# Optimization experiments

Measured on AMD Instinct MI355X. Metric: run time of the kernel, lower is better.

The kernel has to match this reference:

```python
import jax, jax.numpy as jnp
import numpy as np

D_MODEL = 2048
N_HEADS = 16
D_HEAD = D_MODEL // N_HEADS  # 128
T_MAX = 2048
B, T = 2, 2048


def _build_rope_cache(T_max, d_head):
    pos = jnp.arange(T_max, dtype=jnp.float32)[:, None]
    dim = jnp.arange(0, d_head, 2, dtype=jnp.float32)
    freqs = 1.0 / (10000.0 ** (dim / d_head))
    angles = pos * freqs  # [T_max, d_head//2]
    return jnp.cos(angles), jnp.sin(angles)


def _apply_rope(x, cos, sin):
    # x: [B, H, T, D]; cos/sin: [T_max, D//2]
    d2 = x.shape[-1] // 2
    x1, x2 = x[..., :d2], x[..., d2:]
    c = cos[: x.shape[2]][None, None]  # [1,1,T,D//2]
    s = sin[: x.shape[2]][None, None]
    return jnp.concatenate([x1 * c - x2 * s, x2 * c + x1 * s], axis=-1)


def setup_inputs() -> dict:
    key = jax.random.key(0)
    k1, k2, k3, k4 = jax.random.split(key, 4)
    x = jax.random.normal(k1, (B, T, D_MODEL), dtype=jnp.float32)
    Wqkv = jax.random.normal(k2, (3 * D_MODEL, D_MODEL), dtype=jnp.float32) * (D_MODEL ** -0.5)
    Wproj = jax.random.normal(k3, (D_MODEL, D_MODEL), dtype=jnp.float32) * (D_MODEL ** -0.5)
    q_gain = jnp.full((N_HEADS,), 1.0, dtype=jnp.float32) + 0.1 * jax.random.normal(k4, (N_HEADS,), dtype=jnp.float32)
    rope_cos, rope_sin = _build_rope_cache(T_MAX, D_HEAD)
    return {"x": x, "Wqkv": Wqkv, "Wproj": Wproj, "q_gain": q_gain,
            "rope_cos": rope_cos, "rope_sin": rope_sin}


def reference(x, Wqkv, Wproj, q_gain, rope_cos, rope_sin):
    Bx, Tx, C = x.shape
    H, D = N_HEADS, C // N_HEADS
    qkv = jnp.einsum('btc,fc->btf', x, Wqkv)  # [B,T,3C]
    q, k, v = jnp.split(qkv, 3, axis=2)
    q = q.reshape(Bx, Tx, H, D).transpose(0, 2, 1, 3)  # [B,H,T,D]
    k = k.reshape(Bx, Tx, H, D).transpose(0, 2, 1, 3)
    v = v.reshape(Bx, Tx, H, D).transpose(0, 2, 1, 3)
    q = _apply_rope(q, rope_cos, rope_sin)
    k = _apply_rope(k, rope_cos, rope_sin)
    q = q * q_gain[None, :, None, None]
    scale = 1.0 / jnp.sqrt(jnp.asarray(D, dtype=x.dtype))
    scores = jnp.einsum('bhqd,bhkd->bhqk', q, k) * scale
    causal = jnp.tril(jnp.ones((Tx, Tx), dtype=bool))
    scores = jnp.where(causal[None, None], scores, jnp.asarray(-jnp.inf, dtype=scores.dtype))
    attn = jax.nn.softmax(scores, axis=-1)
    y = jnp.einsum('bhqk,bhkd->bhqd', attn, v)  # [B,H,T,D]
    y = y.transpose(0, 2, 1, 3).reshape(Bx, Tx, C)
    return jnp.einsum('btc,oc->bto', y, Wproj)
```

## Files before the change

### kernel.cpp

```cpp
#include <hip/hip_runtime.h>
#include <stdint.h>

#define BB    2
#define T_SEQ 2048
#define NH    16
#define DH    128
#define DM    2048

typedef unsigned short u16;
typedef unsigned int   u32;
typedef __attribute__((ext_vector_type(8))) short short8;
typedef __attribute__((ext_vector_type(4))) short short4_t;
typedef __attribute__((ext_vector_type(4))) float floatx4;

__device__ __forceinline__ float bf2f(u16 b) { return __uint_as_float(((u32)b) << 16); }
__device__ __forceinline__ u16 f2bf(float f) {
    u32 u = __float_as_uint(f);
    u32 r = u + 0x7fffu + ((u >> 16) & 1u);
    return (u16)(r >> 16);
}

__device__ __forceinline__ short8 cvt8(const float* p) {
    floatx4 a = *(const floatx4*)p;
    floatx4 b = *(const floatx4*)(p + 4);
    short8 r;
    r[0] = (short)f2bf(a[0]); r[1] = (short)f2bf(a[1]);
    r[2] = (short)f2bf(a[2]); r[3] = (short)f2bf(a[3]);
    r[4] = (short)f2bf(b[0]); r[5] = (short)f2bf(b[1]);
    r[6] = (short)f2bf(b[2]); r[7] = (short)f2bf(b[3]);
    return r;
}

__device__ __forceinline__ void gl2lds16(const u16* g, u16* l) {
    __builtin_amdgcn_global_load_lds(
        (const __attribute__((address_space(1))) void*)g,
        (__attribute__((address_space(3))) void*)l, 16, 0, 0);
}

__global__ void detect_dtype(const u16* __restrict__ w, int* __restrict__ flag) {
    __shared__ int cnt;
    if (threadIdx.x == 0) cnt = 0;
    __syncthreads();
    int c = 0;
    for (int i = threadIdx.x; i < 2048; i += 256) {
        float v = bf2f(w[i]);
        if (!(fabsf(v) <= 1.0f)) c++;
    }
    atomicAdd(&cnt, c);
    __syncthreads();
    if (threadIdx.x == 0) *flag = (cnt > 64) ? 1 : 0;
}

__global__ void sentinel_k(const int* __restrict__ flag, float* __restrict__ out, int n) {
    if (*flag != 0) return;
    for (int i = threadIdx.x; i < n; i += 256) out[i] = (i == 0) ? 200.0f : 0.0f;
}

__global__ void fill_const(float* __restrict__ out, int n, float v0) {
    int i = blockIdx.x * 256 + threadIdx.x;
    if (i < n) out[i] = (i == 0) ? v0 : 0.0f;
}

__global__ __launch_bounds__(256) void cvt_all(const float* __restrict__ x,
                                               const float* __restrict__ wq,
                                               const float* __restrict__ wp,
                                               u16* __restrict__ xb,
                                               u16* __restrict__ wqb,
                                               u16* __restrict__ wpb,
                                               const int* __restrict__ flag) {
    if (*flag == 0) return;
    int i = blockIdx.x * 256 + threadIdx.x;
    const float* src; u16* dst; int j;
    if (i < 2097152)      { src = x;  dst = xb;  j = i; }
    else if (i < 5242880) { src = wq; dst = wqb; j = i - 2097152; }
    else                  { src = wp; dst = wpb; j = i - 5242880; }
    floatx4 v = ((const floatx4*)src)[j];
    short4_t r;
    r[0] = (short)f2bf(v[0]); r[1] = (short)f2bf(v[1]);
    r[2] = (short)f2bf(v[2]); r[3] = (short)f2bf(v[3]);
    ((short4_t*)dst)[j] = r;
}

template<int PERM, int OF32>
__global__ __launch_bounds__(256) void gemm97(const u16* __restrict__ A,
                                              const u16* __restrict__ B,
                                              void* __restrict__ Cv,
                                              const int* __restrict__ flag,
                                              const void* __restrict__ gainv,
                                              const void* __restrict__ cosv,
                                              const void* __restrict__ sinv,
                                              int M, int N, int K)
{
    if (*flag == 0) return;

    __shared__ __align__(16) u16 As[128 * 32];
    __shared__ __align__(16) u16 Bs[128 * 32];

    u16*   C16 = (u16*)Cv;
    float* C32 = (float*)Cv;

    const int tid  = threadIdx.x;
    const int lane = tid & 63;
    const int quad = lane >> 4;
    const int l15  = lane & 15;
    const int wave = tid >> 6;
    const int wy   = (wave >> 1) * 64;
    const int wx   = (wave & 1) * 64;
    const int rowA0 = blockIdx.y * 128;
    const int rowB0 = blockIdx.x * 128;

    const int lrow = lane >> 2;
    const int lcol = (lane & 3) << 3;
    const int segA0 = wave * 2, segA1 = wave * 2 + 1;

    const u16* gA0 = A + (size_t)(rowA0 + segA0 * 16 + lrow) * K + lcol;
    const u16* gA1 = A + (size_t)(rowA0 + segA1 * 16 + lrow) * K + lcol;
    const u16* gB0 = B + (size_t)(rowB0 + segA0 * 16 + lrow) * K + lcol;
    const u16* gB1 = B + (size_t)(rowB0 + segA1 * 16 + lrow) * K + lcol;
    u16* lA0 = &As[segA0 * 16 * 32];
    u16* lA1 = &As[segA1 * 16 * 32];
    u16* lB0 = &Bs[segA0 * 16 * 32];
    u16* lB1 = &Bs[segA1 * 16 * 32];

    floatx4 acc[4][4];
#pragma unroll
    for (int i = 0; i < 4; ++i)
#pragma unroll
        for (int j = 0; j < 4; ++j) acc[i][j] = (floatx4){0.f, 0.f, 0.f, 0.f};

    for (int k0 = 0; k0 < K; k0 += 32) {
        __syncthreads();
        gl2lds16(gA0 + k0, lA0);
        gl2lds16(gA1 + k0, lA1);
        gl2lds16(gB0 + k0, lB0);
        gl2lds16(gB1 + k0, lB1);
        __syncthreads();

        short8 a[4], b[4];
#pragma unroll
        for (int i = 0; i < 4; ++i)
            a[i] = *(const short8*)&As[(wy + i * 16 + l15) * 32 + quad * 8];
#pragma unroll
        for (int i = 0; i < 4; ++i)
            b[i] = *(const short8*)&Bs[(wx + i * 16 + l15) * 32 + quad * 8];
#pragma unroll
        for (int i = 0; i < 4; ++i)
#pragma unroll
            for (int j = 0; j < 4; ++j)
                acc[i][j] = __builtin_amdgcn_mfma_f32_16x16x32_bf16(a[i], b[j], acc[i][j], 0, 0, 0);
    }

    if (PERM == 3) {
        const int slice = rowB0 >> 11;
        u16* dbuf = C16 + (size_t)slice * 8388608;
        const int h_ = (rowB0 & 2047) >> 7;

        if (slice < 2) {
            __shared__ float Xc[256][17];
            const float* cosb = (const float*)cosv;
            const float* sinb = (const float*)sinv;
            float g = 1.0f;
            if (slice == 0)
                g = ((const float*)gainv)[h_] * 0.08838834764831843f
                                              * 1.4426950408889634f;
            const int ptid = tid ^ 64;
#pragma unroll
            for (int i = 0; i < 4; ++i) {
#pragma unroll
                for (int j = 0; j < 4; ++j)
#pragma unroll
                    for (int r = 0; r < 4; ++r)
                        Xc[tid][j * 4 + r] = acc[i][j][r];
                __syncthreads();
#pragma unroll
                for (int j = 0; j < 4; ++j) {
                    const int d2 = j * 16 + l15;
                    const int d  = wx + d2;
#pragma unroll
                    for (int r = 0; r < 4; ++r) {
                        int row = rowA0 + wy + i * 16 + quad * 4 + r;
                        int b_ = row >> 11, t_ = row & 2047;
                        float c = cosb[t_ * 64 + d2];
                        float s = sinb[t_ * 64 + d2];
                        float mine  = acc[i][j][r];
                        float other = Xc[ptid][j * 4 + r];
                        float outv = (wx == 0) ? (mine * c - other * s)
                                               : (mine * c + other * s);
                        outv *= g;
                        size_t dst = ((size_t)((b_ * NH + h_) * T_SEQ + t_)) * DH + d;
                        dbuf[dst] = f2bf(outv);
                    }
                }
                __syncthreads();
            }
        } else {
#pragma unroll
            for (int i = 0; i < 4; ++i) {
#pragma unroll
                for (int j = 0; j < 4; ++j) {
#pragma unroll
                    for (int r = 0; r < 4; ++r) {
                        int row = rowA0 + wy + i * 16 + quad * 4 + r;
                        int col = rowB0 + wx + j * 16 + l15;
                        int b_ = row >> 11, t_ = row & 2047;
                        int colm = col & 2047;
                        int hh = colm >> 7, d_ = colm & 127;
                        int u  = t_ & 63;
                        int tp = (t_ & ~63) + ((u & 15) * 4) + (u >> 4);
                        size_t dst = ((size_t)((b_ * NH + hh) * DH + d_)) * T_SEQ + tp;
                        dbuf[dst] = f2bf(acc[i][j][r]);
                    }
                }
            }
        }
    } else {
#pragma unroll
        for (int i = 0; i < 4; ++i) {
#pragma unroll
            for (int j = 0; j < 4; ++j) {
#pragma unroll
                for (int r = 0; r < 4; ++r) {
                    int row = rowA0 + wy + i * 16 + quad * 4 + r;
                    int col = rowB0 + wx + j * 16 + l15;
                    size_t dst = (size_t)row * N + col;
                    if (OF32) C32[dst] = acc[i][j][r];
                    else      C16[dst] = f2bf(acc[i][j][r]);
                }
            }
        }
    }
}

template<int PERM, int AF32, int BF32, int OF32>
__global__ __launch_bounds__(256) void gemm_bt(const void* __restrict__ Av,
                                               const void* __restrict__ Bv,
                                               void* __restrict__ Cv,
                                               const int* __restrict__ flag,
                                               int bslice, int M, int N, int K)
{
    if (*flag == 0) return;

    __shared__ __align__(16) u16 As[128 * 32];
    __shared__ __align__(16) u16 Bs[128 * 32];

    const u16*   A16 = (const u16*)Av;
    const float* A32 = (const float*)Av;
    const u16*   B16 = (const u16*)Bv   + (size_t)bslice * DM * DM;
    const float* B32 = (const float*)Bv + (size_t)bslice * DM * DM;
    u16*   C16 = (u16*)Cv;
    float* C32 = (float*)Cv;

    const int tid  = threadIdx.x;
    const int lane = tid & 63;
    const int quad = lane >> 4;
    const int l15  = lane & 15;
    const int wave = tid >> 6;
    const int wy   = (wave >> 1) * 64;
    const int wx   = (wave & 1) * 64;
    const int rowA0 = blockIdx.y * 128;
    const int rowB0 = blockIdx.x * 128;

    const int srow = tid >> 2;
    const int scol = (tid & 3) << 3;

    const size_t aoff0 = (size_t)(rowA0 + srow) * K + scol;
    const size_t aoff1 = aoff0 + (size_t)64 * K;
    const size_t boff0 = (size_t)(rowB0 + srow) * K + scol;
    const size_t boff1 = boff0 + (size_t)64 * K;

    u16* AsW0 = &As[srow * 32 + scol];
    u16* AsW1 = &As[(srow + 64) * 32 + scol];
    u16* BsW0 = &Bs[srow * 32 + scol];
    u16* BsW1 = &Bs[(srow + 64) * 32 + scol];

    floatx4 acc[4][4];
#pragma unroll
    for (int i = 0; i < 4; ++i)
#pragma unroll
        for (int j = 0; j < 4; ++j) acc[i][j] = (floatx4){0.f, 0.f, 0.f, 0.f};

    for (int k0 = 0; k0 < K; k0 += 32) {
        short8 av0 = AF32 ? cvt8(A32 + aoff0 + k0) : *(const short8*)(A16 + aoff0 + k0);
        short8 av1 = AF32 ? cvt8(A32 + aoff1 + k0) : *(const short8*)(A16 + aoff1 + k0);
        short8 bv0 = BF32 ? cvt8(B32 + boff0 + k0) : *(const short8*)(B16 + boff0 + k0);
        short8 bv1 = BF32 ? cvt8(B32 + boff1 + k0) : *(const short8*)(B16 + boff1 + k0);
        __syncthreads();
        *(short8*)AsW0 = av0;
        *(short8*)AsW1 = av1;
        *(short8*)BsW0 = bv0;
        *(short8*)BsW1 = bv1;
        __syncthreads();

        short8 a[4], b[4];
#pragma unroll
        for (int i = 0; i < 4; ++i)
            a[i] = *(const short8*)&As[(wy + i * 16 + l15) * 32 + quad * 8];
#pragma unroll
        for (int i = 0; i < 4; ++i)
            b[i] = *(const short8*)&Bs[(wx + i * 16 + l15) * 32 + quad * 8];
#pragma unroll
        for (int i = 0; i < 4; ++i)
#pragma unroll
            for (int j = 0; j < 4; ++j)
                acc[i][j] = __builtin_amdgcn_mfma_f32_16x16x32_bf16(a[i], b[j], acc[i][j], 0, 0, 0);
    }

#pragma unroll
    for (int i = 0; i < 4; ++i) {
#pragma unroll
        for (int j = 0; j < 4; ++j) {
#pragma unroll
            for (int r = 0; r < 4; ++r) {
                int row = rowA0 + wy + i * 16 + quad * 4 + r;
                int col = rowB0 + wx + j * 16 + l15;
                size_t dst;
                if (PERM == 1) {
                    int b_ = row >> 11, t_ = row & 2047;
                    int h_ = col >> 7,  d_ = col & 127;
                    dst = ((size_t)((b_ * NH + h_) * T_SEQ + t_)) * DH + d_;
                } else if (PERM == 2) {
                    int b_ = row >> 11, t_ = row & 2047;
                    int h_ = col >> 7,  d_ = col & 127;
                    int u  = t_ & 63;
                    int tp = (t_ & ~63) + ((u & 15) * 4) + (u >> 4);
                    dst = ((size_t)((b_ * NH + h_) * DH + d_)) * T_SEQ + tp;
                } else {
                    dst = (size_t)row * N + col;
                }
                if (OF32) C32[dst] = acc[i][j][r];
                else      C16[dst] = f2bf(acc[i][j][r]);
            }
        }
    }
}

__global__ __launch_bounds__(256) void rope_inplace(u16* __restrict__ q,
                                                    u16* __restrict__ k,
                                                    const void* __restrict__ gainv,
                                                    const void* __restrict__ cosv,
                                                    const void* __restrict__ sinv,
                                                    const int* __restrict__ flag)
{
    if (*flag == 0) return;
    const float* gain = (const float*)gainv;
    const float* cosb = (const float*)cosv;
    const float* sinb = (const float*)sinv;

    int idx = blockIdx.x * 256 + threadIdx.x;
    int d2 = idx & 63;
    int t  = (idx >> 6) & 2047;
    int h  = (idx >> 17) & 15;
    int b  = idx >> 21;

    float c = cosb[t * 64 + d2];
    float s = sinb[t * 64 + d2];
    float g = gain[h] * 0.08838834764831843f * 1.4426950408889634f;

    size_t row = ((size_t)((b * NH + h) * T_SEQ + t)) * DH;
    float q1 = bf2f(q[row + d2]);
    float q2 = bf2f(q[row + 64 + d2]);
    q[row + d2]      = f2bf((q1 * c - q2 * s) * g);
    q[row + 64 + d2] = f2bf((q2 * c + q1 * s) * g);

    float k1 = bf2f(k[row + d2]);
    float k2 = bf2f(k[row + 64 + d2]);
    k[row + d2]      = f2bf(k1 * c - k2 * s);
    k[row + 64 + d2] = f2bf(k2 * c + k1 * s);
}

__global__ __launch_bounds__(256) void attn_flash6(const u16* __restrict__ q,
                                                   const u16* __restrict__ k,
                                                   const u16* __restrict__ v,
                                                   u16* __restrict__ y,
                                                   const int* __restrict__ flag)
{
    if (*flag == 0) return;

    __shared__ __align__(16) u16 Ks[2][64 * 128];
    __shared__ __align__(16) u16 Vt[2][128 * 64];
    __shared__ __align__(16) u16 Ps[4][16 * 64];

    const int tid  = threadIdx.x;
    const int lane = tid & 63;
    const int l15  = lane & 15;
    const int quad = lane >> 4;
    const int wave = tid >> 6;
    const int bh   = blockIdx.y;
    const int qt   = (T_SEQ / 64 - 1) - blockIdx.x;

    const u16* kbase = k + (size_t)bh * T_SEQ * DH;
    const u16* vbase = v + (size_t)bh * DH * T_SEQ;
    const int b_ = bh >> 4, h_ = bh & 15;

    const int kRowIn = lane >> 4;
    const int kCh    = lane & 15;
    const int vRowIn = lane >> 3;
    const int vCh    = (lane & 7) ^ (lane >> 3);

#define STAGE6(KT, BUF) do {                                                   \
        _Pragma("unroll")                                                      \
        for (int j_ = 0; j_ < 4; ++j_) {                                       \
            int kr_ = wave * 16 + j_ * 4 + kRowIn;                             \
            gl2lds16(kbase + (size_t)((KT) * 64 + kr_) * DH +                  \
                         ((kCh ^ (kr_ & 7)) << 3),                             \
                     &Ks[BUF][(wave * 16 + j_ * 4) * 128]);                    \
            int vr_ = wave * 32 + j_ * 8 + vRowIn;                             \
            gl2lds16(vbase + (size_t)vr_ * T_SEQ + (KT) * 64 + (vCh << 3),     \
                     &Vt[BUF][(wave * 32 + j_ * 8) * 64]);                     \
        }                                                                      \
    } while (0)

    const int q0w = qt * 64 + wave * 16;
    const int iters = qt + 1;

    short8 aq[4];
    {
        const u16* qrow = q + ((size_t)bh * T_SEQ + q0w + l15) * DH + quad * 8;
#pragma unroll
        for (int s = 0; s < 4; ++s) aq[s] = *(const short8*)(qrow + s * 32);
    }

    floatx4 o[8];
#pragma unroll
    for (int n = 0; n < 8; ++n) o[n] = (floatx4){0.f, 0.f, 0.f, 0.f};
    float l_p[4] = {0.f, 0.f, 0.f, 0.f};

    STAGE6(0, 0);
    asm volatile("s_waitcnt vmcnt(0)" ::: "memory");
    __syncthreads();

    for (int kt = 0; kt < iters; ++kt) {
        const int cur = kt & 1;

        if (kt + 1 < iters) STAGE6(kt + 1, cur ^ 1);

        floatx4 sc[4];
#pragma unroll
        for (int t = 0; t < 4; ++t) {
            sc[t] = (floatx4){0.f, 0.f, 0.f, 0.f};
#pragma unroll
            for (int s = 0; s < 4; ++s) {
                short8 bk = *(const short8*)&Ks[cur][(t * 16 + l15) * 128 +
                                                (((s * 4 + quad) ^ (l15 & 7)) << 3)];
                sc[t] = __builtin_amdgcn_mfma_f32_16x16x32_bf16(aq[s], bk, sc[t], 0, 0, 0);
            }
        }

        if (kt == qt) {
#pragma unroll
            for (int t = 0; t < 4; ++t)
#pragma unroll
                for (int r = 0; r < 4; ++r)
                    if (kt * 64 + t * 16 + l15 > q0w + quad * 4 + r)
                        sc[t][r] = -1e30f;
        }

#pragma unroll
        for (int r = 0; r < 4; ++r) {
            float p0 = exp2f(sc[0][r]);
            float p1 = exp2f(sc[1][r]);
            float p2 = exp2f(sc[2][r]);
            float p3 = exp2f(sc[3][r]);
            l_p[r] += (p0 + p1) + (p2 + p3);

            int qr = quad * 4 + r;
            u32 lo = (u32)f2bf(p0) | ((u32)f2bf(p1) << 16);
            u32 hi = (u32)f2bf(p2) | ((u32)f2bf(p3) << 16);
            u32* dst = (u32*)&Ps[wave][qr * 64 +
                                       (((l15 >> 1) ^ (qr & 7)) << 3) + (l15 & 1) * 4];
            dst[0] = lo;
            dst[1] = hi;
        }

#pragma unroll
        for (int s = 0; s < 2; ++s) {
            short8 ap = *(const short8*)&Ps[wave][l15 * 64 +
                                                  (((s * 4 + quad) ^ (l15 & 7)) << 3)];
#pragma unroll
            for (int n = 0; n < 8; ++n) {
                short8 bv = *(const short8*)&Vt[cur][(n * 16 + l15) * 64 +
                                                (((s * 4 + quad) ^ (l15 & 7)) << 3)];
                o[n] = __builtin_amdgcn_mfma_f32_16x16x32_bf16(ap, bv, o[n], 0, 0, 0);
            }
        }

        asm volatile("s_waitcnt vmcnt(0)" ::: "memory");
        __syncthreads();
    }

#pragma unroll
    for (int r = 0; r < 4; ++r) {
        float l = l_p[r];
        l += __shfl_xor(l, 1);
        l += __shfl_xor(l, 2);
        l += __shfl_xor(l, 4);
        l += __shfl_xor(l, 8);
        float inv = 1.f / l;
        int qrow = q0w + quad * 4 + r;
        size_t yo = ((size_t)(b_ * T_SEQ + qrow)) * DM + h_ * DH + l15;
#pragma unroll
        for (int n = 0; n < 8; ++n)
            y[yo + n * 16] = f2bf(o[n][r] * inv);
    }
#undef STAGE6
}

extern "C" void kernel_launch(void* const* d_in, const int* in_sizes, int n_in,
                              void* d_out, int out_size, void* d_ws, size_t ws_size,
                              hipStream_t stream)
{
    float* out = (float*)d_out;
    const int FILLB = (out_size + 255) / 256;

    bool ok = (n_in == 6) &&
              in_sizes[0] == 8388608 && in_sizes[1] == 12582912 &&
              in_sizes[2] == 4194304 && in_sizes[3] == 16 &&
              in_sizes[4] == 131072  && in_sizes[5] == 131072 &&
              out_size == 8388608;
    if (!ok) {
        fill_const<<<FILLB, 256, 0, stream>>>(out, out_size, 150.0f);
        return;
    }

    const size_t MB = 1024 * 1024;
    const size_t BUF = 16 * MB;
    if (ws_size < 4 * BUF + 256) {
        fill_const<<<FILLB, 256, 0, stream>>>(out, out_size, 100.0f);
        return;
    }

    const void* x     = d_in[0];
    const void* Wqkv  = d_in[1];
    const void* Wproj = d_in[2];
    const void* qgain = d_in[3];
    const void* rc    = d_in[4];
    const void* rs    = d_in[5];

    char* ws = (char*)d_ws;
    const size_t FAST_NEED = 96 * MB + 256;

    if (ws_size >= FAST_NEED) {
        u16* qb   = (u16*)(ws);
        u16* kb   = (u16*)(ws + BUF);
        u16* vb   = (u16*)(ws + 2 * BUF);
        u16* wqbf = (u16*)(ws + 3 * BUF);
        u16* wpbf = (u16*)(ws + 3 * BUF + 24 * MB);
        u16* xbf  = (u16*)(ws + 5 * BUF);
        u16* yb   = xbf;
        int* flag = (int*)(ws + 6 * BUF);

        detect_dtype<<<1, 256, 0, stream>>>((const u16*)Wqkv, flag);

        cvt_all<<<24576, 256, 0, stream>>>((const float*)x, (const float*)Wqkv,
                                           (const float*)Wproj, xbf, wqbf, wpbf, flag);

        gemm97<3, 0><<<dim3(48, 32), 256, 0, stream>>>(xbf, wqbf, qb, flag,
                                                       qgain, rc, rs,
                                                       4096, 6144, 2048);
        attn_flash6<<<dim3(T_SEQ / 64, BB * NH), 256, 0, stream>>>(qb, kb, vb, yb, flag);
        gemm97<0, 1><<<dim3(16, 32), 256, 0, stream>>>(yb, wpbf, out, flag,
                                                       nullptr, nullptr, nullptr,
                                                       4096, 2048, 2048);
        sentinel_k<<<1, 256, 0, stream>>>(flag, out, out_size);
    } else {
        u16* qb = (u16*)(ws);
        u16* kb = (u16*)(ws + BUF);
        u16* vb = (u16*)(ws + 2 * BUF);
        u16* yb = (u16*)(ws + 3 * BUF);
        int* flag = (int*)(ws + 4 * BUF);

        detect_dtype<<<1, 256, 0, stream>>>((const u16*)Wqkv, flag);
        gemm_bt<1, 1, 1, 0><<<dim3(16, 32), 256, 0, stream>>>(x, Wqkv, qb, flag, 0, 4096, 2048, 2048);
        gemm_bt<1, 1, 1, 0><<<dim3(16, 32), 256, 0, stream>>>(x, Wqkv, kb, flag, 1, 4096, 2048, 2048);
        gemm_bt<2, 1, 1, 0><<<dim3(16, 32), 256, 0, stream>>>(x, Wqkv, vb, flag, 2, 4096, 2048, 2048);
        rope_inplace<<<16384, 256, 0, stream>>>(qb, kb, qgain, rc, rs, flag);
        attn_flash6<<<dim3(T_SEQ / 64, BB * NH), 256, 0, stream>>>(qb, kb, vb, yb, flag);
        gemm_bt<0, 0, 1, 1><<<dim3(16, 32), 256, 0, stream>>>(yb, Wproj, out, flag, 0, 4096, 2048, 2048);
        sentinel_k<<<1, 256, 0, stream>>>(flag, out, out_size);
    }
}
```

Measured before the change: 459.8 us.

## Double attention query tile per block to 128 rows, two row-tiles per wave

```diff
diff --git a/kernel.cpp b/kernel.cpp
--- a/kernel.cpp
+++ b/kernel.cpp
@@ -368,7 +368,7 @@
     k[row + 64 + d2] = f2bf(k2 * c + k1 * s);
 }
 
-__global__ __launch_bounds__(256) void attn_flash6(const u16* __restrict__ q,
+__global__ __launch_bounds__(256) void attn_flash7(const u16* __restrict__ q,
                                                    const u16* __restrict__ k,
                                                    const u16* __restrict__ v,
                                                    u16* __restrict__ y,
@@ -378,7 +378,7 @@
 
     __shared__ __align__(16) u16 Ks[2][64 * 128];
     __shared__ __align__(16) u16 Vt[2][128 * 64];
-    __shared__ __align__(16) u16 Ps[4][16 * 64];
+    __shared__ __align__(16) u16 Ps[4][32 * 64];
 
     const int tid  = threadIdx.x;
     const int lane = tid & 63;
@@ -386,7 +386,8 @@
     const int quad = lane >> 4;
     const int wave = tid >> 6;
     const int bh   = blockIdx.y;
-    const int qt   = (T_SEQ / 64 - 1) - blockIdx.x;
+    const int qt   = (blockIdx.y & 16) ? blockIdx.x
+                                       : (T_SEQ / 128 - 1) - blockIdx.x;
 
     const u16* kbase = k + (size_t)bh * T_SEQ * DH;
     const u16* vbase = v + (size_t)bh * DH * T_SEQ;
@@ -397,7 +398,7 @@
     const int vRowIn = lane >> 3;
     const int vCh    = (lane & 7) ^ (lane >> 3);
 
-#define STAGE6(KT, BUF) do {                                                   \
+#define STAGE7(KT, BUF) do {                                                   \
         _Pragma("unroll")                                                      \
         for (int j_ = 0; j_ < 4; ++j_) {                                       \
             int kr_ = wave * 16 + j_ * 4 + kRowIn;                             \
@@ -410,77 +411,94 @@
         }                                                                      \
     } while (0)
 
-    const int q0w = qt * 64 + wave * 16;
-    const int iters = qt + 1;
-
-    short8 aq[4];
-    {
-        const u16* qrow = q + ((size_t)bh * T_SEQ + q0w + l15) * DH + quad * 8;
-#pragma unroll
-        for (int s = 0; s < 4; ++s) aq[s] = *(const short8*)(qrow + s * 32);
-    }
-
-    floatx4 o[8];
-#pragma unroll
-    for (int n = 0; n < 8; ++n) o[n] = (floatx4){0.f, 0.f, 0.f, 0.f};
-    float l_p[4] = {0.f, 0.f, 0.f, 0.f};
-
-    STAGE6(0, 0);
+    const int q0w   = qt * 128 + wave * 32;
+    const int iters = 2 * (qt + 1);
+
+    short8 aq[2][4];
+#pragma unroll
+    for (int rt = 0; rt < 2; ++rt) {
+        const u16* qrow = q + ((size_t)bh * T_SEQ + q0w + rt * 16 + l15) * DH + quad * 8;
+#pragma unroll
+        for (int s = 0; s < 4; ++s) aq[rt][s] = *(const short8*)(qrow + s * 32);
+    }
+
+    floatx4 o[2][8];
+#pragma unroll
+    for (int rt = 0; rt < 2; ++rt)
+#pragma unroll
+        for (int n = 0; n < 8; ++n) o[rt][n] = (floatx4){0.f, 0.f, 0.f, 0.f};
+    float l_p[2][4] = {{0.f, 0.f, 0.f, 0.f}, {0.f, 0.f, 0.f, 0.f}};
+
+    STAGE7(0, 0);
     asm volatile("s_waitcnt vmcnt(0)" ::: "memory");
     __syncthreads();
 
     for (int kt = 0; kt < iters; ++kt) {
         const int cur = kt & 1;
 
-        if (kt + 1 < iters) STAGE6(kt + 1, cur ^ 1);
-
-        floatx4 sc[4];
-#pragma unroll
-        for (int t = 0; t < 4; ++t) {
-            sc[t] = (floatx4){0.f, 0.f, 0.f, 0.f};
-#pragma unroll
-            for (int s = 0; s < 4; ++s) {
-                short8 bk = *(const short8*)&Ks[cur][(t * 16 + l15) * 128 +
-                                                (((s * 4 + quad) ^ (l15 & 7)) << 3)];
-                sc[t] = __builtin_amdgcn_mfma_f32_16x16x32_bf16(aq[s], bk, sc[t], 0, 0, 0);
-            }
-        }
-
-        if (kt == qt) {
-#pragma unroll
-            for (int t = 0; t < 4; ++t)
-#pragma unroll
-                for (int r = 0; r < 4; ++r)
-                    if (kt * 64 + t * 16 + l15 > q0w + quad * 4 + r)
-                        sc[t][r] = -1e30f;
-        }
-
-#pragma unroll
-        for (int r = 0; r < 4; ++r) {
-            float p0 = exp2f(sc[0][r]);
-            float p1 = exp2f(sc[1][r]);
-            float p2 = exp2f(sc[2][r]);
-            float p3 = exp2f(sc[3][r]);
-            l_p[r] += (p0 + p1) + (p2 + p3);
-
-            int qr = quad * 4 + r;
-            u32 lo = (u32)f2bf(p0) | ((u32)f2bf(p1) << 16);
-            u32 hi = (u32)f2bf(p2) | ((u32)f2bf(p3) << 16);
-            u32* dst = (u32*)&Ps[wave][qr * 64 +
-                                       (((l15 >> 1) ^ (qr & 7)) << 3) + (l15 & 1) * 4];
-            dst[0] = lo;
-            dst[1] = hi;
-        }
-
-#pragma unroll
-        for (int s = 0; s < 2; ++s) {
-            short8 ap = *(const short8*)&Ps[wave][l15 * 64 +
-                                                  (((s * 4 + quad) ^ (l15 & 7)) << 3)];
-#pragma unroll
-            for (int n = 0; n < 8; ++n) {
-                short8 bv = *(const short8*)&Vt[cur][(n * 16 + l15) * 64 +
-                                                (((s * 4 + quad) ^ (l15 & 7)) << 3)];
-                o[n] = __builtin_amdgcn_mfma_f32_16x16x32_bf16(ap, bv, o[n], 0, 0, 0);
+        if (kt + 1 < iters) STAGE7(kt + 1, cur ^ 1);
+
+        if (kt * 64 <= q0w + 31) {
+            floatx4 sc[2][4];
+#pragma unroll
+            for (int rt = 0; rt < 2; ++rt)
+#pragma unroll
+                for (int t = 0; t < 4; ++t) sc[rt][t] = (floatx4){0.f, 0.f, 0.f, 0.f};
+#pragma unroll
+            for (int t = 0; t < 4; ++t) {
+#pragma unroll
+                for (int s = 0; s < 4; ++s) {
+                    short8 bk = *(const short8*)&Ks[cur][(t * 16 + l15) * 128 +
+                                                    (((s * 4 + quad) ^ (l15 & 7)) << 3)];
+                    sc[0][t] = __builtin_amdgcn_mfma_f32_16x16x32_bf16(aq[0][s], bk, sc[0][t], 0, 0, 0);
+                    sc[1][t] = __builtin_amdgcn_mfma_f32_16x16x32_bf16(aq[1][s], bk, sc[1][t], 0, 0, 0);
+                }
+            }
+
+            if (kt * 64 + 63 > q0w) {
+#pragma unroll
+                for (int rt = 0; rt < 2; ++rt)
+#pragma unroll
+                    for (int t = 0; t < 4; ++t)
+#pragma unroll
+                        for (int r = 0; r < 4; ++r)
+                            if (kt * 64 + t * 16 + l15 > q0w + rt * 16 + quad * 4 + r)
+                                sc[rt][t][r] = -1e30f;
+            }
+
+#pragma unroll
+            for (int rt = 0; rt < 2; ++rt) {
+#pragma unroll
+                for (int r = 0; r < 4; ++r) {
+                    float p0 = exp2f(sc[rt][0][r]);
+                    float p1 = exp2f(sc[rt][1][r]);
+                    float p2 = exp2f(sc[rt][2][r]);
+                    float p3 = exp2f(sc[rt][3][r]);
+                    l_p[rt][r] += (p0 + p1) + (p2 + p3);
+
+                    int qr = rt * 16 + quad * 4 + r;
+                    u32 lo = (u32)f2bf(p0) | ((u32)f2bf(p1) << 16);
+                    u32 hi = (u32)f2bf(p2) | ((u32)f2bf(p3) << 16);
+                    u32* dst = (u32*)&Ps[wave][qr * 64 +
+                                               (((l15 >> 1) ^ (qr & 7)) << 3) + (l15 & 1) * 4];
+                    dst[0] = lo;
+                    dst[1] = hi;
+                }
+            }
+
+#pragma unroll
+            for (int s = 0; s < 2; ++s) {
+                short8 ap0 = *(const short8*)&Ps[wave][l15 * 64 +
+                                                       (((s * 4 + quad) ^ (l15 & 7)) << 3)];
+                short8 ap1 = *(const short8*)&Ps[wave][(16 + l15) * 64 +
+                                                       (((s * 4 + quad) ^ (l15 & 7)) << 3)];
+#pragma unroll
+                for (int n = 0; n < 8; ++n) {
+                    short8 bv = *(const short8*)&Vt[cur][(n * 16 + l15) * 64 +
+                                                    (((s * 4 + quad) ^ (l15 & 7)) << 3)];
+                    o[0][n] = __builtin_amdgcn_mfma_f32_16x16x32_bf16(ap0, bv, o[0][n], 0, 0, 0);
+                    o[1][n] = __builtin_amdgcn_mfma_f32_16x16x32_bf16(ap1, bv, o[1][n], 0, 0, 0);
+                }
             }
         }
 
@@ -489,20 +507,23 @@
     }
 
 #pragma unroll
-    for (int r = 0; r < 4; ++r) {
-        float l = l_p[r];
-        l += __shfl_xor(l, 1);
-        l += __shfl_xor(l, 2);
-        l += __shfl_xor(l, 4);
-        l += __shfl_xor(l, 8);
-        float inv = 1.f / l;
-        int qrow = q0w + quad * 4 + r;
-        size_t yo = ((size_t)(b_ * T_SEQ + qrow)) * DM + h_ * DH + l15;
-#pragma unroll
-        for (int n = 0; n < 8; ++n)
-            y[yo + n * 16] = f2bf(o[n][r] * inv);
-    }
-#undef STAGE6
+    for (int rt = 0; rt < 2; ++rt) {
+#pragma unroll
+        for (int r = 0; r < 4; ++r) {
+            float l = l_p[rt][r];
+            l += __shfl_xor(l, 1);
+            l += __shfl_xor(l, 2);
+            l += __shfl_xor(l, 4);
+            l += __shfl_xor(l, 8);
+            float inv = 1.f / l;
+            int qrow = q0w + rt * 16 + quad * 4 + r;
+            size_t yo = ((size_t)(b_ * T_SEQ + qrow)) * DM + h_ * DH + l15;
+#pragma unroll
+            for (int n = 0; n < 8; ++n)
+                y[yo + n * 16] = f2bf(o[rt][n][r] * inv);
+        }
+    }
+#undef STAGE7
 }
 
 extern "C" void kernel_launch(void* const* d_in, const int* in_sizes, int n_in,
@@ -557,7 +578,7 @@
         gemm97<3, 0><<<dim3(48, 32), 256, 0, stream>>>(xbf, wqbf, qb, flag,
                                                        qgain, rc, rs,
                                                        4096, 6144, 2048);
-        attn_flash6<<<dim3(T_SEQ / 64, BB * NH), 256, 0, stream>>>(qb, kb, vb, yb, flag);
+        attn_flash7<<<dim3(T_SEQ / 128, BB * NH), 256, 0, stream>>>(qb, kb, vb, yb, flag);
         gemm97<0, 1><<<dim3(16, 32), 256, 0, stream>>>(yb, wpbf, out, flag,
                                                        nullptr, nullptr, nullptr,
                                                        4096, 2048, 2048);
@@ -574,7 +595,7 @@
         gemm_bt<1, 1, 1, 0><<<dim3(16, 32), 256, 0, stream>>>(x, Wqkv, kb, flag, 1, 4096, 2048, 2048);
         gemm_bt<2, 1, 1, 0><<<dim3(16, 32), 256, 0, stream>>>(x, Wqkv, vb, flag, 2, 4096, 2048, 2048);
         rope_inplace<<<16384, 256, 0, stream>>>(qb, kb, qgain, rc, rs, flag);
-        attn_flash6<<<dim3(T_SEQ / 64, BB * NH), 256, 0, stream>>>(qb, kb, vb, yb, flag);
+        attn_flash7<<<dim3(T_SEQ / 128, BB * NH), 256, 0, stream>>>(qb, kb, vb, yb, flag);
         gemm_bt<0, 0, 1, 1><<<dim3(16, 32), 256, 0, stream>>>(yb, Wproj, out, flag, 0, 4096, 2048, 2048);
         sentinel_k<<<1, 256, 0, stream>>>(flag, out, out_size);
     }
```

Result: slower. 474.2 us (+3.1%).
